# Optimization experiments

Measured on AMD Instinct MI355X. Metric: run time of the kernel, lower is better.

The kernel has to match this reference:

```python
import jax, jax.numpy as jnp
import numpy as np

BLOCK_K = 128  # per_1x128 block quantization: block_n=1 (per row), block_k=128


def _dequant(wq, scale):
    # wq: [E, N, K] quantized codes; scale: [E, N, ceil(K/BLOCK_K)]
    K = wq.shape[-1]
    s_full = jnp.repeat(scale, BLOCK_K, axis=-1)[..., :K]
    return wq * s_full


def setup_inputs() -> dict:
    key = jax.random.key(0)
    ks = jax.random.split(key, 6)
    T, E, H, I = 1024, 8, 1024, 768
    x = jax.random.normal(ks[0], (T, H), dtype=jnp.float32)
    router_logits = jax.random.normal(ks[1], (T, E), dtype=jnp.float32)
    # fp8 codes simulated as float values; block scales positive (scale_inv)
    w13_weight = jax.random.normal(ks[2], (E, 2 * I, H), dtype=jnp.float32) * 0.05
    w13_weight_scale_inv = jax.random.uniform(ks[3], (E, 2 * I, H // BLOCK_K), dtype=jnp.float32, minval=0.5, maxval=1.5)
    w2_weight = jax.random.normal(ks[4], (E, H, I), dtype=jnp.float32) * 0.05
    w2_weight_scale_inv = jax.random.uniform(ks[5], (E, H, I // BLOCK_K), dtype=jnp.float32, minval=0.5, maxval=1.5)
    return {
        "x": x,
        "router_logits": router_logits,
        "w13_weight": w13_weight,
        "w13_weight_scale_inv": w13_weight_scale_inv,
        "w2_weight": w2_weight,
        "w2_weight_scale_inv": w2_weight_scale_inv,
        "top_k": 2,
    }


def reference(x, router_logits, w13_weight, w13_weight_scale_inv, w2_weight, w2_weight_scale_inv, top_k):
    T, H = x.shape
    E = router_logits.shape[-1]
    I = w2_weight.shape[-1]

    # ---- dequantize block-scaled weights (inline dequant of fp8 grouped GEMM) ----
    w13 = _dequant(w13_weight, w13_weight_scale_inv)   # [E, 2I, H]
    w2 = _dequant(w2_weight, w2_weight_scale_inv)      # [E, H, I]

    # ---- routing: softmax scoring, top_k, renormalize ----
    probs = jax.nn.softmax(router_logits, axis=-1)     # [T, E]
    topk_w, topk_idx = jax.lax.top_k(probs, top_k)     # [T, K]
    topk_w = topk_w / jnp.sum(topk_w, axis=-1, keepdims=True)  # renormalize=True
    # dense combine weights [T, E] (scatter of top_k routing weights)
    combine = jnp.zeros((T, E), x.dtype).at[jnp.arange(T)[:, None], topk_idx].add(topk_w)

    # ---- grouped expert FFN (dense-over-experts reference) ----
    gate_up = jnp.einsum('th,enh->ten', x, w13)        # [T, E, 2I]
    gate, up = gate_up[..., :I], gate_up[..., I:]
    act = jax.nn.silu(gate) * up                       # silu activation ('silu')
    out_e = jnp.einsum('tei,ehi->teh', act, w2)        # [T, E, H]

    # ---- combine ----
    return jnp.einsum('teh,te->th', out_e, combine)    # [T, H]
```

## Files before the change

kernel.cpp:

```cpp
#include <hip/hip_runtime.h>

#define T_TOK 1024
#define H_DIM 1024
#define I_DIM 768
#define E_NUM 8

#define A_W13 6144
#define A_X   512
#define A_Z   512
#define G13 1572864
#define G2   786432

#define GEMM1_BLOCKS 3072
#define W2DQ_BLOCKS  3072

typedef __bf16 bf16x8 __attribute__((ext_vector_type(8)));
typedef float  f32x4  __attribute__((ext_vector_type(4)));

__device__ inline bf16x8 cvt8(float4 a, float4 b, float s) {
    bf16x8 o;
    o[0] = (__bf16)(a.x * s); o[1] = (__bf16)(a.y * s);
    o[2] = (__bf16)(a.z * s); o[3] = (__bf16)(a.w * s);
    o[4] = (__bf16)(b.x * s); o[5] = (__bf16)(b.y * s);
    o[6] = (__bf16)(b.z * s); o[7] = (__bf16)(b.w * s);
    return o;
}

__global__ __launch_bounds__(256) void prep13_kernel(
    const float* __restrict__ w13, const float* __restrict__ w13s,
    const float* __restrict__ x,   float4* __restrict__ out4,
    __bf16* __restrict__ w13d,     __bf16* __restrict__ xbf,
    const float* __restrict__ logits,
    int* __restrict__ counts, int* __restrict__ base,
    int* __restrict__ tok_list, float* __restrict__ wt_list)
{
    const int bx = blockIdx.x;
    if (bx < A_W13) {
        int g = bx * 256 + threadIdx.x;
        int k8 = g & 127;
        int row = g >> 7;
        float s = w13s[(row << 3) | (k8 >> 4)];
        const float4* src = (const float4*)w13 + (size_t)g * 2;
        *(bf16x8*)(w13d + (size_t)g * 8) = cvt8(src[0], src[1], s);
        return;
    }
    if (bx < A_W13 + A_X) {
        int g = (bx - A_W13) * 256 + threadIdx.x;
        const float4* src = (const float4*)x + (size_t)g * 2;
        *(bf16x8*)(xbf + (size_t)g * 8) = cvt8(src[0], src[1], 1.0f);
        return;
    }
    if (bx < A_W13 + A_X + A_Z) {
        int go = (bx - A_W13 - A_X) * 256 + threadIdx.x;
        float4 z = make_float4(0.f, 0.f, 0.f, 0.f);
        out4[2 * go] = z; out4[2 * go + 1] = z;
        return;
    }
    __shared__ int cnt[E_NUM];
    const int t0 = threadIdx.x;
    if (t0 < E_NUM) cnt[t0] = 0;
    __syncthreads();
#pragma unroll
    for (int tt = 0; tt < 4; tt++) {
        int t = t0 + tt * 256;
        float l[E_NUM];
#pragma unroll
        for (int e = 0; e < E_NUM; e++) l[e] = logits[t * E_NUM + e];
        int e0 = 0; float m0 = l[0];
#pragma unroll
        for (int e = 1; e < E_NUM; e++) if (l[e] > m0) { m0 = l[e]; e0 = e; }
        int e1 = -1; float m1 = -3e38f;
#pragma unroll
        for (int e = 0; e < E_NUM; e++) if (e != e0 && l[e] > m1) { m1 = l[e]; e1 = e; }
        float w0 = 1.0f / (1.0f + expf(m1 - m0));
        float w1 = 1.0f - w0;
        int p0 = atomicAdd(&cnt[e0], 1);
        tok_list[e0 * T_TOK + p0] = t;
        wt_list[e0 * T_TOK + p0] = w0;
        int p1 = atomicAdd(&cnt[e1], 1);
        tok_list[e1 * T_TOK + p1] = t;
        wt_list[e1 * T_TOK + p1] = w1;
    }
    __syncthreads();
    if (t0 == 0) {
        int s = 0;
        for (int e = 0; e < E_NUM; e++) { base[e] = s; counts[e] = cnt[e]; s += cnt[e]; }
    }
}

#define MFMA(A, B, C) __builtin_amdgcn_mfma_f32_16x16x32_bf16(A, B, C, 0, 0, 0)

struct Stage { uint4 a0, b0, b1, b2, b3; };

__device__ inline Stage ld_stage(const __bf16* pA0, const __bf16* pB, int k) {
    Stage s;
    s.a0 = *(const uint4*)(pA0 + k);
    s.b0 = *(const uint4*)(pB + k);
    s.b1 = *(const uint4*)(pB + k + 8);
    s.b2 = *(const uint4*)(pB + k + 16);
    s.b3 = *(const uint4*)(pB + k + 24);
    return s;
}

__device__ inline void st_stage(char* As, char* Bs, int aw0,
                                int bw0, int bw1, int bw2, int bw3,
                                const Stage& s) {
    *(uint4*)(As + aw0) = s.a0;
    *(uint4*)(Bs + bw0) = s.b0;
    *(uint4*)(Bs + bw1) = s.b1;
    *(uint4*)(Bs + bw2) = s.b2;
    *(uint4*)(Bs + bw3) = s.b3;
}

__global__ __launch_bounds__(256, 3) void gemm1_kernel(
    const __bf16* __restrict__ xbf,
    const __bf16* __restrict__ w13d,
    const int* __restrict__ counts,
    const int* __restrict__ base,
    const int* __restrict__ tok_list,
    __bf16* __restrict__ act,
    const float* __restrict__ w2,
    const float* __restrict__ w2s,
    __bf16* __restrict__ w2d)
{
    const int bx = blockIdx.x;
    if (bx >= GEMM1_BLOCKS) {
        int g2 = (bx - GEMM1_BLOCKS) * 256 + threadIdx.x;
        unsigned row = (unsigned)g2 / 96u;
        int k8 = g2 - row * 96;
        float s = w2s[row * 6 + (k8 >> 4)];
        const float4* src = (const float4*)w2 + (size_t)g2 * 2;
        *(bf16x8*)(w2d + (size_t)g2 * 8) = cvt8(src[0], src[1], s);
        return;
    }

    const int xcd = bx & 7, t = bx >> 3;
    const int m = t & 31, p = t >> 5;
    const int P = xcd + 8 * p;
    const int nb = P % 12, e = P / 12;
    const int count = counts[e];
    const int m0 = m * 32;
    if (m0 >= count) return;
    const int n0 = nb * 64;
    const int abase = base[e];

    __shared__ union {
        struct { __bf16 Bs[2][128 * 64]; __bf16 As[2][32 * 64]; } s;
        float gu[32 * 132];
    } u;
    __shared__ int tokS[32];

    const int tid = threadIdx.x;
    if (tid < 32) {
        int r = m0 + tid;
        tokS[tid] = (r < count) ? tok_list[e * T_TOK + r] : tok_list[e * T_TOK];
    }
    __syncthreads();

    const int arow = tid >> 3, ag = tid & 7;
    const __bf16* pA0 = xbf + (size_t)tokS[arow] * H_DIM + ag * 8;
    const int aw0 = arow * 128 + ((ag ^ (arow & 7)) << 4);
    const int brow = tid >> 1, bg0 = (tid & 1) * 4;
    const int nB = (brow < 64) ? (n0 + brow) : (I_DIM + n0 + brow - 64);
    const __bf16* pB = w13d + ((size_t)e * 2 * I_DIM + nB) * H_DIM + bg0 * 8;
    const int bw0 = brow * 128 + (((bg0 + 0) ^ (brow & 7)) << 4);
    const int bw1 = brow * 128 + (((bg0 + 1) ^ (brow & 7)) << 4);
    const int bw2 = brow * 128 + (((bg0 + 2) ^ (brow & 7)) << 4);
    const int bw3 = brow * 128 + (((bg0 + 3) ^ (brow & 7)) << 4);

    const int wid = tid >> 6, lane = tid & 63, lrow = lane & 15, quad = lane >> 4;
    int aoff[2][2], boff[2][2];
#pragma unroll
    for (int kk = 0; kk < 2; kk++) {
        int gph = ((kk * 4 + quad) ^ (lrow & 7)) << 4;
#pragma unroll
        for (int i = 0; i < 2; i++) aoff[kk][i] = (i * 16 + lrow) * 128 + gph;
#pragma unroll
        for (int j = 0; j < 2; j++) boff[kk][j] = (wid * 32 + j * 16 + lrow) * 128 + gph;
    }

    f32x4 acc[2][2];
#pragma unroll
    for (int i = 0; i < 2; i++)
#pragma unroll
        for (int j = 0; j < 2; j++) { f32x4 z = {0.f, 0.f, 0.f, 0.f}; acc[i][j] = z; }

    char* A0 = (char*)u.s.As[0]; char* A1 = (char*)u.s.As[1];
    char* B0 = (char*)u.s.Bs[0]; char* B1 = (char*)u.s.Bs[1];

    auto compute = [&](const char* Ab, const char* Bb) {
#pragma unroll
        for (int kk = 0; kk < 2; kk++) {
            bf16x8 b0 = *(const bf16x8*)(Bb + boff[kk][0]);
            bf16x8 b1 = *(const bf16x8*)(Bb + boff[kk][1]);
#pragma unroll
            for (int i = 0; i < 2; i++) {
                bf16x8 a = *(const bf16x8*)(Ab + aoff[kk][i]);
                acc[i][0] = MFMA(a, b0, acc[i][0]);
                acc[i][1] = MFMA(a, b1, acc[i][1]);
            }
        }
    };

    Stage X = ld_stage(pA0, pB, 0);
    Stage Y = ld_stage(pA0, pB, 64);
    st_stage(A0, B0, aw0, bw0, bw1, bw2, bw3, X);
    X = ld_stage(pA0, pB, 2 * 64);
    __syncthreads();

#pragma unroll
    for (int uu = 0; uu < 8; ++uu) {
        st_stage(A1, B1, aw0, bw0, bw1, bw2, bw3, Y);
        if (2 * uu + 3 < 16) Y = ld_stage(pA0, pB, (2 * uu + 3) * 64);
        compute(A0, B0);
        __syncthreads();
        if (uu < 7) st_stage(A0, B0, aw0, bw0, bw1, bw2, bw3, X);
        if (2 * uu + 4 < 16) X = ld_stage(pA0, pB, (2 * uu + 4) * 64);
        compute(A1, B1);
        __syncthreads();
    }

#pragma unroll
    for (int i = 0; i < 2; i++)
#pragma unroll
        for (int j = 0; j < 2; j++)
#pragma unroll
            for (int r = 0; r < 4; r++) {
                int mr = i * 16 + quad * 4 + r;
                int c = wid * 32 + j * 16 + lrow;
                u.gu[mr * 132 + c] = acc[i][j][r];
            }
    __syncthreads();

#pragma unroll
    for (int ii = 0; ii < 8; ii++) {
        int o = ii * 256 + tid;
        int mr = o >> 6, c = o & 63;
        if (m0 + mr < count) {
            float g  = u.gu[mr * 132 + c];
            float up = u.gu[mr * 132 + 64 + c];
            float a  = g / (1.0f + expf(-g)) * up;
            act[(size_t)(abase + m0 + mr) * I_DIM + n0 + c] = (__bf16)a;
        }
    }
}

__global__ __launch_bounds__(256, 3) void gemm2_kernel(
    const __bf16* __restrict__ act,
    const __bf16* __restrict__ w2d,
    const int* __restrict__ counts,
    const int* __restrict__ base,
    const int* __restrict__ tok_list,
    const float* __restrict__ wt_list,
    float* __restrict__ out)
{
    const int bx = blockIdx.x;
    const int xcd = bx & 7, t = bx >> 3;
    const int m = t & 31, p = t >> 5;
    const int P = xcd + 8 * p;
    const int nb = P & 7, e = P >> 3;
    const int count = counts[e];
    const int m0 = m * 32;
    if (m0 >= count) return;
    const int n0 = nb * 128;
    const int abase = base[e];

    __shared__ struct { __bf16 Bs[2][128 * 64]; __bf16 As[2][32 * 64]; } s;

    const int tid = threadIdx.x;
    const int arow = tid >> 3, ag = tid & 7;
    int gr0 = abase + m0 + arow;      if (gr0 > 2 * T_TOK - 1) gr0 = 2 * T_TOK - 1;
    const __bf16* pA0 = act + (size_t)gr0 * I_DIM + ag * 8;
    const int aw0 = arow * 128 + ((ag ^ (arow & 7)) << 4);

    const int brow = tid >> 1, bg0 = (tid & 1) * 4;
    const __bf16* pB = w2d + ((size_t)e * H_DIM + n0 + brow) * I_DIM + bg0 * 8;
    const int bw0 = brow * 128 + (((bg0 + 0) ^ (brow & 7)) << 4);
    const int bw1 = brow * 128 + (((bg0 + 1) ^ (brow & 7)) << 4);
    const int bw2 = brow * 128 + (((bg0 + 2) ^ (brow & 7)) << 4);
    const int bw3 = brow * 128 + (((bg0 + 3) ^ (brow & 7)) << 4);

    const int wid = tid >> 6, lane = tid & 63, lrow = lane & 15, quad = lane >> 4;
    int aoff[2][2], boff[2][2];
#pragma unroll
    for (int kk = 0; kk < 2; kk++) {
        int gph = ((kk * 4 + quad) ^ (lrow & 7)) << 4;
#pragma unroll
        for (int i = 0; i < 2; i++) aoff[kk][i] = (i * 16 + lrow) * 128 + gph;
#pragma unroll
        for (int j = 0; j < 2; j++) boff[kk][j] = (wid * 32 + j * 16 + lrow) * 128 + gph;
    }

    f32x4 acc[2][2];
#pragma unroll
    for (int i = 0; i < 2; i++)
#pragma unroll
        for (int j = 0; j < 2; j++) { f32x4 z = {0.f, 0.f, 0.f, 0.f}; acc[i][j] = z; }

    char* A0 = (char*)s.As[0]; char* A1 = (char*)s.As[1];
    char* B0 = (char*)s.Bs[0]; char* B1 = (char*)s.Bs[1];

    auto compute = [&](const char* Ab, const char* Bb) {
#pragma unroll
        for (int kk = 0; kk < 2; kk++) {
            bf16x8 b0 = *(const bf16x8*)(Bb + boff[kk][0]);
            bf16x8 b1 = *(const bf16x8*)(Bb + boff[kk][1]);
#pragma unroll
            for (int i = 0; i < 2; i++) {
                bf16x8 a = *(const bf16x8*)(Ab + aoff[kk][i]);
                acc[i][0] = MFMA(a, b0, acc[i][0]);
                acc[i][1] = MFMA(a, b1, acc[i][1]);
            }
        }
    };

    Stage X = ld_stage(pA0, pB, 0);
    Stage Y = ld_stage(pA0, pB, 64);
    st_stage(A0, B0, aw0, bw0, bw1, bw2, bw3, X);
    X = ld_stage(pA0, pB, 2 * 64);
    __syncthreads();

#pragma unroll
    for (int uu = 0; uu < 6; ++uu) {
        st_stage(A1, B1, aw0, bw0, bw1, bw2, bw3, Y);
        if (2 * uu + 3 < 12) Y = ld_stage(pA0, pB, (2 * uu + 3) * 64);
        compute(A0, B0);
        __syncthreads();
        if (uu < 5) st_stage(A0, B0, aw0, bw0, bw1, bw2, bw3, X);
        if (2 * uu + 4 < 12) X = ld_stage(pA0, pB, (2 * uu + 4) * 64);
        compute(A1, B1);
        __syncthreads();
    }

#pragma unroll
    for (int i = 0; i < 2; i++)
#pragma unroll
        for (int r = 0; r < 4; r++) {
            int mr = i * 16 + quad * 4 + r;
            if (m0 + mr < count) {
                int   tk = tok_list[e * T_TOK + m0 + mr];
                float w  = wt_list[e * T_TOK + m0 + mr];
#pragma unroll
                for (int j = 0; j < 2; j++) {
                    int h = n0 + wid * 32 + j * 16 + lrow;
                    atomicAdd(&out[(size_t)tk * H_DIM + h], w * acc[i][j][r]);
                }
            }
        }
}

extern "C" void kernel_launch(void* const* d_in, const int* in_sizes, int n_in,
                              void* d_out, int out_size, void* d_ws, size_t ws_size,
                              hipStream_t stream) {
    (void)in_sizes; (void)n_in; (void)out_size; (void)ws_size;
    const float* x      = (const float*)d_in[0];
    const float* logits = (const float*)d_in[1];
    const float* w13    = (const float*)d_in[2];
    const float* w13s   = (const float*)d_in[3];
    const float* w2     = (const float*)d_in[4];
    const float* w2s    = (const float*)d_in[5];
    float* out = (float*)d_out;

    char* ws = (char*)d_ws;
    int*    counts   = (int*)ws;
    int*    base     = (int*)(ws + 128);
    int*    tok_list = (int*)(ws + 256);
    float*  wt_list  = (float*)(ws + 256 + 32768);
    __bf16* act      = (__bf16*)(ws + 65792);
    __bf16* xbf      = (__bf16*)(ws + 65792 + 3145728);
    __bf16* w13d     = (__bf16*)(ws + 65792 + 3145728 + 2097152);
    __bf16* w2d      = (__bf16*)(ws + 65792 + 3145728 + 2097152 + 25165824);

    prep13_kernel<<<dim3(A_W13 + A_X + A_Z + 1), 256, 0, stream>>>(
        w13, w13s, x, (float4*)out, w13d, xbf,
        logits, counts, base, tok_list, wt_list);
    gemm1_kernel<<<dim3(GEMM1_BLOCKS + W2DQ_BLOCKS), 256, 0, stream>>>(
        xbf, w13d, counts, base, tok_list, act, w2, w2s, w2d);
    gemm2_kernel<<<dim3(2048), 256, 0, stream>>>(
        act, w2d, counts, base, tok_list, wt_list, out);
}
```

Baseline: 164.7 us.

## Use async global-to-LDS triple-buffered ring and 64-row M tiles in grouped GEMMs

Both grouped GEMM kernels now load their tiles with global_load_lds, which writes straight into shared memory. The loads go into a three-slot ring, and explicit vmcnt waits replace the old register-staged double buffer. The M tile grows from 32 to 64 rows, which halves the GEMM block counts and doubles B-tile reuse per block. This cuts register staging traffic and improves overlap, but occupancy drops to 2 blocks per CU and partially filled 64-row tiles waste more MFMA work when expert counts are uneven.

```diff
diff --git a/kernel.cpp b/kernel.cpp
--- a/kernel.cpp
+++ b/kernel.cpp
@@ -11,8 +11,11 @@
 #define G13 1572864
 #define G2   786432
 
-#define GEMM1_BLOCKS 3072
+#define GEMM1_BLOCKS 1536
 #define W2DQ_BLOCKS  3072
+
+#define SLOT 24576
+#define A_OFF 16384
 
 typedef __bf16 bf16x8 __attribute__((ext_vector_type(8)));
 typedef float  f32x4  __attribute__((ext_vector_type(4)));
@@ -25,6 +28,16 @@
     o[6] = (__bf16)(b.z * s); o[7] = (__bf16)(b.w * s);
     return o;
 }
+
+__device__ inline void async16(const void* g, void* l) {
+    __builtin_amdgcn_global_load_lds(
+        (const __attribute__((address_space(1))) unsigned int*)g,
+        (__attribute__((address_space(3))) unsigned int*)l, 16, 0, 0);
+}
+
+#define VM_WAIT12 asm volatile("s_waitcnt vmcnt(12)" ::: "memory")
+#define VM_WAIT6  asm volatile("s_waitcnt vmcnt(6)"  ::: "memory")
+#define VM_WAIT0  asm volatile("s_waitcnt vmcnt(0)"  ::: "memory")
 
 __global__ __launch_bounds__(256) void prep13_kernel(
     const float* __restrict__ w13, const float* __restrict__ w13s,
@@ -90,29 +103,9 @@
 
 #define MFMA(A, B, C) __builtin_amdgcn_mfma_f32_16x16x32_bf16(A, B, C, 0, 0, 0)
 
-struct Stage { uint4 a0, b0, b1, b2, b3; };
-
-__device__ inline Stage ld_stage(const __bf16* pA0, const __bf16* pB, int k) {
-    Stage s;
-    s.a0 = *(const uint4*)(pA0 + k);
-    s.b0 = *(const uint4*)(pB + k);
-    s.b1 = *(const uint4*)(pB + k + 8);
-    s.b2 = *(const uint4*)(pB + k + 16);
-    s.b3 = *(const uint4*)(pB + k + 24);
-    return s;
-}
-
-__device__ inline void st_stage(char* As, char* Bs, int aw0,
-                                int bw0, int bw1, int bw2, int bw3,
-                                const Stage& s) {
-    *(uint4*)(As + aw0) = s.a0;
-    *(uint4*)(Bs + bw0) = s.b0;
-    *(uint4*)(Bs + bw1) = s.b1;
-    *(uint4*)(Bs + bw2) = s.b2;
-    *(uint4*)(Bs + bw3) = s.b3;
-}
-
-__global__ __launch_bounds__(256, 3) void gemm1_kernel(
+struct StgEnt { const char* p; int l; };
+
+__global__ __launch_bounds__(256, 2) void gemm1_kernel(
     const __bf16* __restrict__ xbf,
     const __bf16* __restrict__ w13d,
     const int* __restrict__ counts,
@@ -135,66 +128,76 @@
     }
 
     const int xcd = bx & 7, t = bx >> 3;
-    const int m = t & 31, p = t >> 5;
+    const int p = t % 12, m = t / 12;
     const int P = xcd + 8 * p;
     const int nb = P % 12, e = P / 12;
     const int count = counts[e];
-    const int m0 = m * 32;
+    const int m0 = m * 64;
     if (m0 >= count) return;
     const int n0 = nb * 64;
     const int abase = base[e];
 
-    __shared__ union {
-        struct { __bf16 Bs[2][128 * 64]; __bf16 As[2][32 * 64]; } s;
-        float gu[32 * 132];
-    } u;
-    __shared__ int tokS[32];
+    __shared__ union { uint4 r4[3 * SLOT / 16]; float gu[64 * 132]; } u;
+    __shared__ int tokS[64];
+    char* ring = (char*)u.r4;
 
     const int tid = threadIdx.x;
-    if (tid < 32) {
+    if (tid < 64) {
         int r = m0 + tid;
         tokS[tid] = (r < count) ? tok_list[e * T_TOK + r] : tok_list[e * T_TOK];
     }
     __syncthreads();
 
-    const int arow = tid >> 3, ag = tid & 7;
-    const __bf16* pA0 = xbf + (size_t)tokS[arow] * H_DIM + ag * 8;
-    const int aw0 = arow * 128 + ((ag ^ (arow & 7)) << 4);
-    const int brow = tid >> 1, bg0 = (tid & 1) * 4;
-    const int nB = (brow < 64) ? (n0 + brow) : (I_DIM + n0 + brow - 64);
-    const __bf16* pB = w13d + ((size_t)e * 2 * I_DIM + nB) * H_DIM + bg0 * 8;
-    const int bw0 = brow * 128 + (((bg0 + 0) ^ (brow & 7)) << 4);
-    const int bw1 = brow * 128 + (((bg0 + 1) ^ (brow & 7)) << 4);
-    const int bw2 = brow * 128 + (((bg0 + 2) ^ (brow & 7)) << 4);
-    const int bw3 = brow * 128 + (((bg0 + 3) ^ (brow & 7)) << 4);
-
-    const int wid = tid >> 6, lane = tid & 63, lrow = lane & 15, quad = lane >> 4;
-    int aoff[2][2], boff[2][2];
+    const int wv = tid >> 6, ln = tid & 63;
+    StgEnt se[6];
+#pragma unroll
+    for (int j = 0; j < 6; j++) {
+        int off = wv * 6144 + j * 1024 + ln * 16;
+        se[j].l = wv * 6144 + j * 1024;
+        if (off < A_OFF) {
+            int r = off >> 7, sl = (off >> 4) & 7, g = sl ^ (r & 7);
+            int nB = (r < 64) ? (n0 + r) : (I_DIM + n0 + r - 64);
+            se[j].p = (const char*)w13d + ((size_t)e * 2 * I_DIM + nB) * 2048 + g * 16;
+        } else {
+            int ao = off - A_OFF, r = ao >> 7, sl = (ao >> 4) & 7, g = sl ^ (r & 7);
+            se[j].p = (const char*)xbf + (size_t)tokS[r] * 2048 + g * 16;
+        }
+    }
+
+#define ISSUE(kc, sb) do { \
+        async16(se[0].p + (kc) * 128, (sb) + se[0].l); \
+        async16(se[1].p + (kc) * 128, (sb) + se[1].l); \
+        async16(se[2].p + (kc) * 128, (sb) + se[2].l); \
+        async16(se[3].p + (kc) * 128, (sb) + se[3].l); \
+        async16(se[4].p + (kc) * 128, (sb) + se[4].l); \
+        async16(se[5].p + (kc) * 128, (sb) + se[5].l); } while (0)
+
+    const int wid = wv, lane = ln, lrow = lane & 15, quad = lane >> 4;
+    int aoff[2][4], boff[2][2];
 #pragma unroll
     for (int kk = 0; kk < 2; kk++) {
         int gph = ((kk * 4 + quad) ^ (lrow & 7)) << 4;
 #pragma unroll
-        for (int i = 0; i < 2; i++) aoff[kk][i] = (i * 16 + lrow) * 128 + gph;
+        for (int i = 0; i < 4; i++) aoff[kk][i] = (i * 16 + lrow) * 128 + gph;
 #pragma unroll
         for (int j = 0; j < 2; j++) boff[kk][j] = (wid * 32 + j * 16 + lrow) * 128 + gph;
     }
 
-    f32x4 acc[2][2];
-#pragma unroll
-    for (int i = 0; i < 2; i++)
+    f32x4 acc[4][2];
+#pragma unroll
+    for (int i = 0; i < 4; i++)
 #pragma unroll
         for (int j = 0; j < 2; j++) { f32x4 z = {0.f, 0.f, 0.f, 0.f}; acc[i][j] = z; }
 
-    char* A0 = (char*)u.s.As[0]; char* A1 = (char*)u.s.As[1];
-    char* B0 = (char*)u.s.Bs[0]; char* B1 = (char*)u.s.Bs[1];
-
-    auto compute = [&](const char* Ab, const char* Bb) {
+    auto compute = [&](const char* sb) {
+        const char* Bb = sb;
+        const char* Ab = sb + A_OFF;
 #pragma unroll
         for (int kk = 0; kk < 2; kk++) {
             bf16x8 b0 = *(const bf16x8*)(Bb + boff[kk][0]);
             bf16x8 b1 = *(const bf16x8*)(Bb + boff[kk][1]);
 #pragma unroll
-            for (int i = 0; i < 2; i++) {
+            for (int i = 0; i < 4; i++) {
                 bf16x8 a = *(const bf16x8*)(Ab + aoff[kk][i]);
                 acc[i][0] = MFMA(a, b0, acc[i][0]);
                 acc[i][1] = MFMA(a, b1, acc[i][1]);
@@ -202,26 +205,21 @@
         }
     };
 
-    Stage X = ld_stage(pA0, pB, 0);
-    Stage Y = ld_stage(pA0, pB, 64);
-    st_stage(A0, B0, aw0, bw0, bw1, bw2, bw3, X);
-    X = ld_stage(pA0, pB, 2 * 64);
-    __syncthreads();
-
-#pragma unroll
-    for (int uu = 0; uu < 8; ++uu) {
-        st_stage(A1, B1, aw0, bw0, bw1, bw2, bw3, Y);
-        if (2 * uu + 3 < 16) Y = ld_stage(pA0, pB, (2 * uu + 3) * 64);
-        compute(A0, B0);
-        __syncthreads();
-        if (uu < 7) st_stage(A0, B0, aw0, bw0, bw1, bw2, bw3, X);
-        if (2 * uu + 4 < 16) X = ld_stage(pA0, pB, (2 * uu + 4) * 64);
-        compute(A1, B1);
-        __syncthreads();
-    }
-
-#pragma unroll
-    for (int i = 0; i < 2; i++)
+    ISSUE(0, ring);
+    ISSUE(1, ring + SLOT);
+#pragma unroll
+    for (int k = 0; k < 16; k++) {
+        if (k + 2 < 16) ISSUE(k + 2, ring + ((k + 2) % 3) * SLOT);
+        if (k < 14)       { VM_WAIT12; }
+        else if (k == 14) { VM_WAIT6; }
+        else              { VM_WAIT0; }
+        __builtin_amdgcn_s_barrier();
+        compute(ring + (k % 3) * SLOT);
+        __builtin_amdgcn_s_barrier();
+    }
+
+#pragma unroll
+    for (int i = 0; i < 4; i++)
 #pragma unroll
         for (int j = 0; j < 2; j++)
 #pragma unroll
@@ -233,7 +231,7 @@
     __syncthreads();
 
 #pragma unroll
-    for (int ii = 0; ii < 8; ii++) {
+    for (int ii = 0; ii < 16; ii++) {
         int o = ii * 256 + tid;
         int mr = o >> 6, c = o & 63;
         if (m0 + mr < count) {
@@ -243,9 +241,10 @@
             act[(size_t)(abase + m0 + mr) * I_DIM + n0 + c] = (__bf16)a;
         }
     }
-}
-
-__global__ __launch_bounds__(256, 3) void gemm2_kernel(
+#undef ISSUE
+}
+
+__global__ __launch_bounds__(256, 2) void gemm2_kernel(
     const __bf16* __restrict__ act,
     const __bf16* __restrict__ w2d,
     const int* __restrict__ counts,
@@ -256,57 +255,70 @@
 {
     const int bx = blockIdx.x;
     const int xcd = bx & 7, t = bx >> 3;
-    const int m = t & 31, p = t >> 5;
+    const int p = t & 7, m = t >> 3;
     const int P = xcd + 8 * p;
     const int nb = P & 7, e = P >> 3;
     const int count = counts[e];
-    const int m0 = m * 32;
+    const int m0 = m * 64;
     if (m0 >= count) return;
     const int n0 = nb * 128;
     const int abase = base[e];
 
-    __shared__ struct { __bf16 Bs[2][128 * 64]; __bf16 As[2][32 * 64]; } s;
+    __shared__ uint4 r4[3 * SLOT / 16];
+    char* ring = (char*)r4;
 
     const int tid = threadIdx.x;
-    const int arow = tid >> 3, ag = tid & 7;
-    int gr0 = abase + m0 + arow;      if (gr0 > 2 * T_TOK - 1) gr0 = 2 * T_TOK - 1;
-    const __bf16* pA0 = act + (size_t)gr0 * I_DIM + ag * 8;
-    const int aw0 = arow * 128 + ((ag ^ (arow & 7)) << 4);
-
-    const int brow = tid >> 1, bg0 = (tid & 1) * 4;
-    const __bf16* pB = w2d + ((size_t)e * H_DIM + n0 + brow) * I_DIM + bg0 * 8;
-    const int bw0 = brow * 128 + (((bg0 + 0) ^ (brow & 7)) << 4);
-    const int bw1 = brow * 128 + (((bg0 + 1) ^ (brow & 7)) << 4);
-    const int bw2 = brow * 128 + (((bg0 + 2) ^ (brow & 7)) << 4);
-    const int bw3 = brow * 128 + (((bg0 + 3) ^ (brow & 7)) << 4);
-
-    const int wid = tid >> 6, lane = tid & 63, lrow = lane & 15, quad = lane >> 4;
-    int aoff[2][2], boff[2][2];
+    const int wv = tid >> 6, ln = tid & 63;
+
+    StgEnt se[6];
+#pragma unroll
+    for (int j = 0; j < 6; j++) {
+        int off = wv * 6144 + j * 1024 + ln * 16;
+        se[j].l = wv * 6144 + j * 1024;
+        if (off < A_OFF) {
+            int r = off >> 7, sl = (off >> 4) & 7, g = sl ^ (r & 7);
+            se[j].p = (const char*)w2d + ((size_t)e * H_DIM + n0 + r) * 1536 + g * 16;
+        } else {
+            int ao = off - A_OFF, r = ao >> 7, sl = (ao >> 4) & 7, g = sl ^ (r & 7);
+            int gr = abase + m0 + r; if (gr > 2 * T_TOK - 1) gr = 2 * T_TOK - 1;
+            se[j].p = (const char*)act + (size_t)gr * 1536 + g * 16;
+        }
+    }
+
+#define ISSUE(kc, sb) do { \
+        async16(se[0].p + (kc) * 128, (sb) + se[0].l); \
+        async16(se[1].p + (kc) * 128, (sb) + se[1].l); \
+        async16(se[2].p + (kc) * 128, (sb) + se[2].l); \
+        async16(se[3].p + (kc) * 128, (sb) + se[3].l); \
+        async16(se[4].p + (kc) * 128, (sb) + se[4].l); \
+        async16(se[5].p + (kc) * 128, (sb) + se[5].l); } while (0)
+
+    const int wid = wv, lane = ln, lrow = lane & 15, quad = lane >> 4;
+    int aoff[2][4], boff[2][2];
 #pragma unroll
     for (int kk = 0; kk < 2; kk++) {
         int gph = ((kk * 4 + quad) ^ (lrow & 7)) << 4;
 #pragma unroll
-        for (int i = 0; i < 2; i++) aoff[kk][i] = (i * 16 + lrow) * 128 + gph;
+        for (int i = 0; i < 4; i++) aoff[kk][i] = (i * 16 + lrow) * 128 + gph;
 #pragma unroll
         for (int j = 0; j < 2; j++) boff[kk][j] = (wid * 32 + j * 16 + lrow) * 128 + gph;
     }
 
-    f32x4 acc[2][2];
-#pragma unroll
-    for (int i = 0; i < 2; i++)
+    f32x4 acc[4][2];
+#pragma unroll
+    for (int i = 0; i < 4; i++)
 #pragma unroll
         for (int j = 0; j < 2; j++) { f32x4 z = {0.f, 0.f, 0.f, 0.f}; acc[i][j] = z; }
 
-    char* A0 = (char*)s.As[0]; char* A1 = (char*)s.As[1];
-    char* B0 = (char*)s.Bs[0]; char* B1 = (char*)s.Bs[1];
-
-    auto compute = [&](const char* Ab, const char* Bb) {
+    auto compute = [&](const char* sb) {
+        const char* Bb = sb;
+        const char* Ab = sb + A_OFF;
 #pragma unroll
         for (int kk = 0; kk < 2; kk++) {
             bf16x8 b0 = *(const bf16x8*)(Bb + boff[kk][0]);
             bf16x8 b1 = *(const bf16x8*)(Bb + boff[kk][1]);
 #pragma unroll
-            for (int i = 0; i < 2; i++) {
+            for (int i = 0; i < 4; i++) {
                 bf16x8 a = *(const bf16x8*)(Ab + aoff[kk][i]);
                 acc[i][0] = MFMA(a, b0, acc[i][0]);
                 acc[i][1] = MFMA(a, b1, acc[i][1]);
@@ -314,26 +326,21 @@
         }
     };
 
-    Stage X = ld_stage(pA0, pB, 0);
-    Stage Y = ld_stage(pA0, pB, 64);
-    st_stage(A0, B0, aw0, bw0, bw1, bw2, bw3, X);
-    X = ld_stage(pA0, pB, 2 * 64);
-    __syncthreads();
-
-#pragma unroll
-    for (int uu = 0; uu < 6; ++uu) {
-        st_stage(A1, B1, aw0, bw0, bw1, bw2, bw3, Y);
-        if (2 * uu + 3 < 12) Y = ld_stage(pA0, pB, (2 * uu + 3) * 64);
-        compute(A0, B0);
-        __syncthreads();
-        if (uu < 5) st_stage(A0, B0, aw0, bw0, bw1, bw2, bw3, X);
-        if (2 * uu + 4 < 12) X = ld_stage(pA0, pB, (2 * uu + 4) * 64);
-        compute(A1, B1);
-        __syncthreads();
-    }
-
-#pragma unroll
-    for (int i = 0; i < 2; i++)
+    ISSUE(0, ring);
+    ISSUE(1, ring + SLOT);
+#pragma unroll
+    for (int k = 0; k < 12; k++) {
+        if (k + 2 < 12) ISSUE(k + 2, ring + ((k + 2) % 3) * SLOT);
+        if (k < 10)       { VM_WAIT12; }
+        else if (k == 10) { VM_WAIT6; }
+        else              { VM_WAIT0; }
+        __builtin_amdgcn_s_barrier();
+        compute(ring + (k % 3) * SLOT);
+        __builtin_amdgcn_s_barrier();
+    }
+
+#pragma unroll
+    for (int i = 0; i < 4; i++)
 #pragma unroll
         for (int r = 0; r < 4; r++) {
             int mr = i * 16 + quad * 4 + r;
@@ -347,6 +354,7 @@
                 }
             }
         }
+#undef ISSUE
 }
 
 extern "C" void kernel_launch(void* const* d_in, const int* in_sizes, int n_in,
@@ -376,6 +384,6 @@
         logits, counts, base, tok_list, wt_list);
     gemm1_kernel<<<dim3(GEMM1_BLOCKS + W2DQ_BLOCKS), 256, 0, stream>>>(
         xbf, w13d, counts, base, tok_list, act, w2, w2s, w2d);
-    gemm2_kernel<<<dim3(2048), 256, 0, stream>>>(
+    gemm2_kernel<<<dim3(1024), 256, 0, stream>>>(
         act, w2d, counts, base, tok_list, wt_list, out);
 }
```

After: 154.7 us. -6.1%, faster.
